# Optimization experiments

Hardware: AMD Instinct MI355X
Metric: run time of the kernel (lower is better)

## Reference

```python
import jax, jax.numpy as jnp
import numpy as np

B, N, L, D_IN, D = 32, 2048, 32768, 4, 64


def setup_inputs() -> dict:
    key = jax.random.key(0)
    ks = jax.random.split(key, 10)
    s = 0.05  # modest init scale for params
    return {
        "pred_node": jax.random.normal(ks[0], (B, N, D_IN), jnp.float32),
        "line_param": jax.random.normal(ks[1], (B, L, 4), jnp.float32),
        "W_embed": jax.random.normal(ks[2], (D_IN, D), jnp.float32) * s,
        "b_embed": jnp.zeros((D,), jnp.float32),
        "W1": jax.random.normal(ks[3], (2 * D, D), jnp.float32) * s,
        "b1": jnp.zeros((D,), jnp.float32),
        "W2": jax.random.normal(ks[4], (D, 4), jnp.float32) * s,
        "b2": jnp.zeros((4,), jnp.float32),
        "edge_src": jax.random.randint(ks[5], (B, L), 0, N, jnp.int32),
        "edge_dst": jax.random.randint(ks[6], (B, L), 0, N, jnp.int32),
    }


def reference(pred_node, line_param, W_embed, b_embed, W1, b1, W2, b2,
              edge_src, edge_dst):
    # node_feat_to_line_feat: Linear(4 -> d_model) over all nodes at once
    node_feat = jnp.einsum("bni,id->bnd", pred_node, W_embed) + b_embed  # (B,N,D)

    # Batched gather of node-feature pairs per edge (replaces Python loops)
    fi = jnp.take_along_axis(node_feat, edge_src[..., None].astype(jnp.int32), axis=1)  # (B,L,D)
    fj = jnp.take_along_axis(node_feat, edge_dst[..., None].astype(jnp.int32), axis=1)  # (B,L,D)
    combined = jnp.concatenate([fi, fj], axis=-1)  # (B,L,2D)

    # line_pred_head: Linear(2D->D) -> ReLU -> Dropout(eval: identity) -> Linear(D->4)
    h = jax.nn.relu(jnp.einsum("ble,ed->bld", combined, W1) + b1)
    line_pred = jnp.einsum("bld,do->blo", h, W2) + b2  # (B,L,4)

    # Cols 0,1 copied from line_param; cols 2,3 from the prediction head
    out = jnp.concatenate([line_param[..., :2], line_pred[..., 2:4]], axis=-1)
    return out
```

## Files before the change

### kernel.cpp

```cpp
#include <hip/hip_runtime.h>
#include <stdint.h>

#define B_ 32
#define N_ 2048
#define L_ 32768


__global__ void prep_kernel(const float* __restrict__ W_embed,
                            const float* __restrict__ b_embed,
                            const float* __restrict__ W1,
                            const float* __restrict__ b1,
                            const float* __restrict__ W2,
                            float* __restrict__ wc) {
    int d = threadIdx.x;
    float acc1[4] = {0.f, 0.f, 0.f, 0.f};
    float acc2[4] = {0.f, 0.f, 0.f, 0.f};
    float bb = 0.f;
    for (int k = 0; k < 64; ++k) {
        float w1a = W1[k * 64 + d];
        float w1b = W1[(64 + k) * 64 + d];
        float be = b_embed[k];
        bb = fmaf(be, w1a + w1b, bb);
#pragma unroll
        for (int i = 0; i < 4; ++i) {
            float we = W_embed[i * 64 + k];
            acc1[i] = fmaf(we, w1a, acc1[i]);
            acc2[i] = fmaf(we, w1b, acc2[i]);
        }
    }
    float* w = wc + d * 12;
#pragma unroll
    for (int i = 0; i < 4; ++i) {
        w[i] = acc1[i];
        w[4 + i] = acc2[i];
    }
    w[8] = bb + b1[d];
    w[9] = W2[d * 4 + 2];
    w[10] = W2[d * 4 + 3];
    w[11] = 0.f;
}

__global__ __launch_bounds__(256, 4) void edge_kernel(
    const float4* __restrict__ pred_node,
    const float* __restrict__ wc,
    const int* __restrict__ esrc, const int* __restrict__ edst,
    const float2* __restrict__ lp2,
    const float* __restrict__ b2,
    float4* __restrict__ out) {
    __shared__ float4 spn[N_];

    int tid = threadIdx.x;
    int bid = blockIdx.x;
    int x = bid & 7;
    int i = bid >> 3;
    int b = x + 8 * (i >> 5);
    int j = i & 31;

    const float4* pnb = pred_node + b * N_;
#pragma unroll
    for (int q = 0; q < 8; ++q) {
        int idx = tid + q * 256;
        spn[idx] = pnb[idx];
    }

    int ebase = b * L_ + j * 1024 + tid;

    int sa[4], ta[4];
#pragma unroll
    for (int p = 0; p < 4; ++p) {
        sa[p] = esrc[ebase + p * 256];
        ta[p] = edst[ebase + p * 256];
    }
    float bias2 = b2[2], bias3 = b2[3];

    __syncthreads();

    float4 ps[4], pt[4];
#pragma unroll
    for (int p = 0; p < 4; ++p) {
        ps[p] = spn[sa[p]];
        pt[p] = spn[ta[p]];
    }

    float a2[4] = {bias2, bias2, bias2, bias2};
    float a3[4] = {bias3, bias3, bias3, bias3};

    const float4* wq = (const float4*)wc;
#pragma unroll 1
    for (int fc = 0; fc < 16; ++fc) {
#pragma unroll
        for (int f = 0; f < 4; ++f) {
            int fi = fc * 4 + f;
            float4 wa = wq[fi * 3 + 0];
            float4 wb = wq[fi * 3 + 1];
            float4 wx = wq[fi * 3 + 2];
#pragma unroll
            for (int p = 0; p < 4; ++p) {
                float h = wx.x;
                h = fmaf(ps[p].x, wa.x, h);
                h = fmaf(ps[p].y, wa.y, h);
                h = fmaf(ps[p].z, wa.z, h);
                h = fmaf(ps[p].w, wa.w, h);
                h = fmaf(pt[p].x, wb.x, h);
                h = fmaf(pt[p].y, wb.y, h);
                h = fmaf(pt[p].z, wb.z, h);
                h = fmaf(pt[p].w, wb.w, h);
                h = fmaxf(h, 0.f);
                a2[p] = fmaf(h, wx.y, a2[p]);
                a3[p] = fmaf(h, wx.z, a3[p]);
            }
        }
    }

#pragma unroll
    for (int p = 0; p < 4; ++p) {
        int e = ebase + p * 256;
        float2 v = lp2[(size_t)e * 2];
        out[e] = make_float4(v.x, v.y, a2[p], a3[p]);
    }
}

extern "C" void kernel_launch(void* const* d_in, const int* in_sizes, int n_in,
                              void* d_out, int out_size, void* d_ws, size_t ws_size,
                              hipStream_t stream) {
    const float* pred_node = (const float*)d_in[0];
    const float* line_param = (const float*)d_in[1];
    const float* W_embed = (const float*)d_in[2];
    const float* b_embed = (const float*)d_in[3];
    const float* W1 = (const float*)d_in[4];
    const float* b1 = (const float*)d_in[5];
    const float* W2 = (const float*)d_in[6];
    const float* b2 = (const float*)d_in[7];
    const int* esrc = (const int*)d_in[8];
    const int* edst = (const int*)d_in[9];
    float* out = (float*)d_out;

    float* wc = (float*)d_ws;

    prep_kernel<<<1, 64, 0, stream>>>(W_embed, b_embed, W1, b1, W2, wc);
    edge_kernel<<<1024, 256, 0, stream>>>((const float4*)pred_node, wc,
                                          esrc, edst,
                                          (const float2*)line_param, b2,
                                          (float4*)out);
}
```

Measured before the change: 115.5 us.

## Process eight edges per thread, prefetch line params, parallelize weight prep

New measurement: 115.2 us. No clear change (-0.2%).

```diff
diff --git a/kernel.cpp b/kernel.cpp
--- a/kernel.cpp
+++ b/kernel.cpp
@@ -6,41 +6,37 @@
 #define L_ 32768
 
 
-__global__ void prep_kernel(const float* __restrict__ W_embed,
-                            const float* __restrict__ b_embed,
-                            const float* __restrict__ W1,
-                            const float* __restrict__ b1,
-                            const float* __restrict__ W2,
-                            float* __restrict__ wc) {
-    int d = threadIdx.x;
-    float acc1[4] = {0.f, 0.f, 0.f, 0.f};
-    float acc2[4] = {0.f, 0.f, 0.f, 0.f};
-    float bb = 0.f;
+__global__ __launch_bounds__(512) void prep_kernel(
+    const float* __restrict__ W_embed, const float* __restrict__ b_embed,
+    const float* __restrict__ W1, const float* __restrict__ b1,
+    const float* __restrict__ W2, float* __restrict__ wc) {
+    int tid = threadIdx.x;
+    int d = tid & 63;
+    int i = (tid >> 6) & 3;
+    int half = tid >> 8;
+
+    const float* w1base = W1 + (half ? 64 * 64 : 0);
+    float acc = 0.f;
+#pragma unroll
     for (int k = 0; k < 64; ++k) {
-        float w1a = W1[k * 64 + d];
-        float w1b = W1[(64 + k) * 64 + d];
-        float be = b_embed[k];
-        bb = fmaf(be, w1a + w1b, bb);
+        acc = fmaf(W_embed[i * 64 + k], w1base[k * 64 + d], acc);
+    }
+    wc[d * 12 + half * 4 + i] = acc;
+
+    if (tid < 64) {
+        float bb = 0.f;
 #pragma unroll
-        for (int i = 0; i < 4; ++i) {
-            float we = W_embed[i * 64 + k];
-            acc1[i] = fmaf(we, w1a, acc1[i]);
-            acc2[i] = fmaf(we, w1b, acc2[i]);
+        for (int k = 0; k < 64; ++k) {
+            bb = fmaf(b_embed[k], W1[k * 64 + d] + W1[(64 + k) * 64 + d], bb);
         }
+        wc[d * 12 + 8] = bb + b1[d];
+        wc[d * 12 + 9] = W2[d * 4 + 2];
+        wc[d * 12 + 10] = W2[d * 4 + 3];
+        wc[d * 12 + 11] = 0.f;
     }
-    float* w = wc + d * 12;
-#pragma unroll
-    for (int i = 0; i < 4; ++i) {
-        w[i] = acc1[i];
-        w[4 + i] = acc2[i];
-    }
-    w[8] = bb + b1[d];
-    w[9] = W2[d * 4 + 2];
-    w[10] = W2[d * 4 + 3];
-    w[11] = 0.f;
 }
 
-__global__ __launch_bounds__(256, 4) void edge_kernel(
+__global__ __launch_bounds__(256, 2) void edge_kernel(
     const float4* __restrict__ pred_node,
     const float* __restrict__ wc,
     const int* __restrict__ esrc, const int* __restrict__ edst,
@@ -53,8 +49,8 @@
     int bid = blockIdx.x;
     int x = bid & 7;
     int i = bid >> 3;
-    int b = x + 8 * (i >> 5);
-    int j = i & 31;
+    int b = x + 8 * (i >> 4);
+    int j = i & 15;
 
     const float4* pnb = pred_node + b * N_;
 #pragma unroll
@@ -63,30 +59,34 @@
         spn[idx] = pnb[idx];
     }
 
-    int ebase = b * L_ + j * 1024 + tid;
+    int ebase = b * L_ + j * 2048 + tid;
 
-    int sa[4], ta[4];
+    int sa[8], ta[8];
+    float2 lp[8];
 #pragma unroll
-    for (int p = 0; p < 4; ++p) {
-        sa[p] = esrc[ebase + p * 256];
-        ta[p] = edst[ebase + p * 256];
+    for (int p = 0; p < 8; ++p) {
+        int e = ebase + p * 256;
+        sa[p] = esrc[e];
+        ta[p] = edst[e];
+        lp[p] = lp2[(size_t)e * 2];
     }
     float bias2 = b2[2], bias3 = b2[3];
 
     __syncthreads();
 
-    float4 ps[4], pt[4];
+    float4 ps[8], pt[8];
 #pragma unroll
-    for (int p = 0; p < 4; ++p) {
+    for (int p = 0; p < 8; ++p) {
         ps[p] = spn[sa[p]];
         pt[p] = spn[ta[p]];
     }
 
-    float a2[4] = {bias2, bias2, bias2, bias2};
-    float a3[4] = {bias3, bias3, bias3, bias3};
+    float a2[8], a3[8];
+#pragma unroll
+    for (int p = 0; p < 8; ++p) { a2[p] = bias2; a3[p] = bias3; }
 
     const float4* wq = (const float4*)wc;
-#pragma unroll 1
+#pragma unroll 2
     for (int fc = 0; fc < 16; ++fc) {
 #pragma unroll
         for (int f = 0; f < 4; ++f) {
@@ -95,7 +95,7 @@
             float4 wb = wq[fi * 3 + 1];
             float4 wx = wq[fi * 3 + 2];
 #pragma unroll
-            for (int p = 0; p < 4; ++p) {
+            for (int p = 0; p < 8; ++p) {
                 float h = wx.x;
                 h = fmaf(ps[p].x, wa.x, h);
                 h = fmaf(ps[p].y, wa.y, h);
@@ -113,10 +113,9 @@
     }
 
 #pragma unroll
-    for (int p = 0; p < 4; ++p) {
+    for (int p = 0; p < 8; ++p) {
         int e = ebase + p * 256;
-        float2 v = lp2[(size_t)e * 2];
-        out[e] = make_float4(v.x, v.y, a2[p], a3[p]);
+        out[e] = make_float4(lp[p].x, lp[p].y, a2[p], a3[p]);
     }
 }
 
@@ -137,9 +136,9 @@
 
     float* wc = (float*)d_ws;
 
-    prep_kernel<<<1, 64, 0, stream>>>(W_embed, b_embed, W1, b1, W2, wc);
-    edge_kernel<<<1024, 256, 0, stream>>>((const float4*)pred_node, wc,
-                                          esrc, edst,
-                                          (const float2*)line_param, b2,
-                                          (float4*)out);
+    prep_kernel<<<1, 512, 0, stream>>>(W_embed, b_embed, W1, b1, W2, wc);
+    edge_kernel<<<512, 256, 0, stream>>>((const float4*)pred_node, wc,
+                                         esrc, edst,
+                                         (const float2*)line_param, b2,
+                                         (float4*)out);
 }
```
